# Kernel tuning notes

Hardware: AMD Instinct MI355X
Metric: run time of the kernel (lower is better)

The kernel has to match this reference:

```python
import jax, jax.numpy as jnp
import numpy as np

B, S, D, E, TOP_K = 4, 4096, 2048, 64, 2


def setup_inputs() -> dict:
    key = jax.random.key(0)
    kx, kw, kb = jax.random.split(key, 3)
    x = jax.random.normal(kx, (B, S, D), dtype=jnp.float32)
    # nn.Linear(d_model, n_expert): weight (E, D), bias (E,)
    bound = 1.0 / np.sqrt(D)
    W = jax.random.uniform(kw, (E, D), dtype=jnp.float32, minval=-bound, maxval=bound)
    b = jax.random.uniform(kb, (E,), dtype=jnp.float32, minval=-bound, maxval=bound)
    return {"x": x, "W": W, "b": b}


def reference(x, W, b):
    # logits: (B, S, E)
    logits = jnp.einsum("bsd,ed->bse", x, W) + b
    top_k_logits, ids = jax.lax.top_k(logits, TOP_K)  # (B,S,K) each
    # scatter top-k logits into a -inf filled tensor along the expert dim
    n = B * S
    flat = jnp.full((n, E), -jnp.inf, dtype=logits.dtype)
    rows = jnp.arange(n)[:, None]  # (n,1)
    flat = flat.at[rows, ids.reshape(n, TOP_K)].set(top_k_logits.reshape(n, TOP_K))
    sparse_logits = flat.reshape(B, S, E)
    router_output = jax.nn.softmax(sparse_logits, axis=-1)  # zeros outside top-k
    return router_output, ids
```

## Files before the change

### kernel.cpp

```cpp
#include <hip/hip_runtime.h>
#include <math.h>

#define NTOK 16384
#define D_   2048
#define E_   64
#define TPB  16
#define NKC  (D_/32)

typedef _Float16 f16x8 __attribute__((ext_vector_type(8)));
typedef float    f32x4 __attribute__((ext_vector_type(4)));

#define LSCALE      256.0f
#define LSCALE2_INV (1.0f/65536.0f)

__global__ __launch_bounds__(256)
void prep_w(const float* __restrict__ W,
            _Float16* __restrict__ wh, _Float16* __restrict__ wl)
{
    const int idx = blockIdx.x * 256 + threadIdx.x;
    const int l  = idx & 63;
    const int kc = (idx >> 6) & 63;
    const int nt = idx >> 12;
    const int e  = nt * 16 + (l & 15);
    const int g  = l >> 4;
    const float* src = W + (size_t)e * D_ + kc * 32 + g * 4;
    const float4 f0 = *reinterpret_cast<const float4*>(src);
    const float4 f1 = *reinterpret_cast<const float4*>(src + 16);
    const float v[8] = {f0.x, f0.y, f0.z, f0.w, f1.x, f1.y, f1.z, f1.w};
    f16x8 h, lo;
#pragma unroll
    for (int j = 0; j < 8; ++j) {
        const float vs = v[j] * LSCALE;
        const _Float16 hj = (_Float16)vs;
        h[j]  = hj;
        lo[j] = (_Float16)(vs - (float)hj);
    }
    *reinterpret_cast<f16x8*>(wh + (size_t)idx * 8) = h;
    *reinterpret_cast<f16x8*>(wl + (size_t)idx * 8) = lo;
}

__global__ __launch_bounds__(64, 1)
void router_mfma(const float* __restrict__ x,
                 const _Float16* __restrict__ wh,
                 const _Float16* __restrict__ wl,
                 const float* __restrict__ bias,
                 float* __restrict__ out)
{
    __shared__ float smem[TPB * 65 + TPB * 4];

    const int l  = threadIdx.x;
    const int T0 = blockIdx.x * TPB;
    const int g  = l >> 4;

    const float* xp = x + (size_t)(T0 + (l & 15)) * D_ + g * 4;
    const _Float16* bh_b = wh + (size_t)l * 8;
    const _Float16* bl_b = wl + (size_t)l * 8;

    f32x4 acc0 = {0.f,0.f,0.f,0.f}, acc1 = {0.f,0.f,0.f,0.f};
    f32x4 acc2 = {0.f,0.f,0.f,0.f}, acc3 = {0.f,0.f,0.f,0.f};

    float4 xa[4], xb[4];
    f16x8  BH[4][4], BL[4][4];

#pragma unroll
    for (int j = 0; j < 4; ++j) {
        xa[j] = *reinterpret_cast<const float4*>(xp + j * 32);
        xb[j] = *reinterpret_cast<const float4*>(xp + j * 32 + 16);
#pragma unroll
        for (int nt = 0; nt < 4; ++nt) {
            BH[j][nt] = *reinterpret_cast<const f16x8*>(bh_b + nt * 32768 + j * 512);
            BL[j][nt] = *reinterpret_cast<const f16x8*>(bl_b + nt * 32768 + j * 512);
        }
    }

    for (int s = 0; s < 16; ++s) {
        const int K = s << 2;
#pragma unroll
        for (int j = 0; j < 4; ++j) {
            f16x8 ah, al_;
            {
                float vs;
                vs = xa[j].x * LSCALE; ah[0] = (_Float16)vs; al_[0] = (_Float16)(vs - (float)ah[0]);
                vs = xa[j].y * LSCALE; ah[1] = (_Float16)vs; al_[1] = (_Float16)(vs - (float)ah[1]);
                vs = xa[j].z * LSCALE; ah[2] = (_Float16)vs; al_[2] = (_Float16)(vs - (float)ah[2]);
                vs = xa[j].w * LSCALE; ah[3] = (_Float16)vs; al_[3] = (_Float16)(vs - (float)ah[3]);
                vs = xb[j].x * LSCALE; ah[4] = (_Float16)vs; al_[4] = (_Float16)(vs - (float)ah[4]);
                vs = xb[j].y * LSCALE; ah[5] = (_Float16)vs; al_[5] = (_Float16)(vs - (float)ah[5]);
                vs = xb[j].z * LSCALE; ah[6] = (_Float16)vs; al_[6] = (_Float16)(vs - (float)ah[6]);
                vs = xb[j].w * LSCALE; ah[7] = (_Float16)vs; al_[7] = (_Float16)(vs - (float)ah[7]);
            }
            acc0 = __builtin_amdgcn_mfma_f32_16x16x32_f16(ah,  BH[j][0], acc0, 0, 0, 0);
            acc0 = __builtin_amdgcn_mfma_f32_16x16x32_f16(al_, BH[j][0], acc0, 0, 0, 0);
            acc0 = __builtin_amdgcn_mfma_f32_16x16x32_f16(ah,  BL[j][0], acc0, 0, 0, 0);
            acc1 = __builtin_amdgcn_mfma_f32_16x16x32_f16(ah,  BH[j][1], acc1, 0, 0, 0);
            acc1 = __builtin_amdgcn_mfma_f32_16x16x32_f16(al_, BH[j][1], acc1, 0, 0, 0);
            acc1 = __builtin_amdgcn_mfma_f32_16x16x32_f16(ah,  BL[j][1], acc1, 0, 0, 0);
            acc2 = __builtin_amdgcn_mfma_f32_16x16x32_f16(ah,  BH[j][2], acc2, 0, 0, 0);
            acc2 = __builtin_amdgcn_mfma_f32_16x16x32_f16(al_, BH[j][2], acc2, 0, 0, 0);
            acc2 = __builtin_amdgcn_mfma_f32_16x16x32_f16(ah,  BL[j][2], acc2, 0, 0, 0);
            acc3 = __builtin_amdgcn_mfma_f32_16x16x32_f16(ah,  BH[j][3], acc3, 0, 0, 0);
            acc3 = __builtin_amdgcn_mfma_f32_16x16x32_f16(al_, BH[j][3], acc3, 0, 0, 0);
            acc3 = __builtin_amdgcn_mfma_f32_16x16x32_f16(ah,  BL[j][3], acc3, 0, 0, 0);
            if (s < 15) {
                const int kn = K + j + 4;
                xa[j] = *reinterpret_cast<const float4*>(xp + kn * 32);
                xb[j] = *reinterpret_cast<const float4*>(xp + kn * 32 + 16);
#pragma unroll
                for (int nt = 0; nt < 4; ++nt) {
                    BH[j][nt] = *reinterpret_cast<const f16x8*>(bh_b + nt * 32768 + (size_t)kn * 512);
                    BL[j][nt] = *reinterpret_cast<const f16x8*>(bl_b + nt * 32768 + (size_t)kn * 512);
                }
            }
        }
    }

    {
        const int col = l & 15;
#pragma unroll
        for (int r = 0; r < 4; ++r) {
            const int t = g * 4 + r;
            smem[t * 65 + 0  + col] = acc0[r] * LSCALE2_INV;
            smem[t * 65 + 16 + col] = acc1[r] * LSCALE2_INV;
            smem[t * 65 + 32 + col] = acc2[r] * LSCALE2_INV;
            smem[t * 65 + 48 + col] = acc3[r] * LSCALE2_INV;
        }
    }
    __syncthreads();

    float* res = smem + TPB * 65;
    if (l < TPB) {
        const float* lg = smem + l * 65;
        float m1 = -INFINITY, m2 = -INFINITY;
        int i1 = 0, i2 = 0;
        for (int e = 0; e < E_; ++e) {
            const float v = lg[e] + bias[e];
            if (v > m1)      { m2 = m1; i2 = i1; m1 = v; i1 = e; }
            else if (v > m2) { m2 = v;  i2 = e; }
        }
        const float ex  = expf(m2 - m1);
        const float den = 1.f + ex;
        res[l*4+0] = 1.f / den;
        res[l*4+1] = ex / den;
        res[l*4+2] = (float)i1;
        res[l*4+3] = (float)i2;
    }
    __syncthreads();

    float* ob = out + (size_t)T0 * E_;
#pragma unroll
    for (int i = 0; i < 4; ++i) {
        const int idx = i * 256 + l * 4;
        const int t   = idx >> 6;
        const int e0  = idx & 63;
        const float p1 = res[t*4+0];
        const float p2 = res[t*4+1];
        const int   i1 = (int)res[t*4+2];
        const int   i2 = (int)res[t*4+3];
        float4 v;
        v.x = (e0+0 == i1) ? p1 : ((e0+0 == i2) ? p2 : 0.f);
        v.y = (e0+1 == i1) ? p1 : ((e0+1 == i2) ? p2 : 0.f);
        v.z = (e0+2 == i1) ? p1 : ((e0+2 == i2) ? p2 : 0.f);
        v.w = (e0+3 == i1) ? p1 : ((e0+3 == i2) ? p2 : 0.f);
        *reinterpret_cast<float4*>(ob + idx) = v;
    }
    if (l < TPB * 2) {
        out[(size_t)NTOK * E_ + (size_t)T0 * 2 + l] =
            res[(l >> 1) * 4 + 2 + (l & 1)];
    }
}

extern "C" void kernel_launch(void* const* d_in, const int* in_sizes, int n_in,
                              void* d_out, int out_size, void* d_ws, size_t ws_size,
                              hipStream_t stream) {
    const float* x = (const float*)d_in[0];
    const float* W = (const float*)d_in[1];
    const float* b = (const float*)d_in[2];
    float* out     = (float*)d_out;
    _Float16* wh   = (_Float16*)d_ws;
    _Float16* wl   = wh + (size_t)4 * NKC * 64 * 8;

    hipLaunchKernelGGL(prep_w, dim3(64), dim3(256), 0, stream, W, wh, wl);
    hipLaunchKernelGGL(router_mfma, dim3(NTOK / TPB), dim3(64), 0, stream,
                       x, wh, wl, b, out);
}
```

Baseline: 51.60 us.

## Split expert tiles across four waves per block instead of one wave

Each block now has four wavefronts, and each wave computes one 16-expert column tile for the block's 16 tokens instead of a single wave computing all four tiles. This cuts per-thread register use (fewer B fragments and accumulators) and raises parallelism per token block. In exchange, every wave reloads and re-splits the same x rows, so x traffic from L1/L2 and conversion work become four times larger. The last loop iteration is peeled so the prefetch no longer needs a branch.

```diff
diff --git a/kernel.cpp b/kernel.cpp
--- a/kernel.cpp
+++ b/kernel.cpp
@@ -39,7 +39,7 @@
     *reinterpret_cast<f16x8*>(wl + (size_t)idx * 8) = lo;
 }
 
-__global__ __launch_bounds__(64, 1)
+__global__ __launch_bounds__(256, 4)
 void router_mfma(const float* __restrict__ x,
                  const _Float16* __restrict__ wh,
                  const _Float16* __restrict__ wl,
@@ -48,32 +48,30 @@
 {
     __shared__ float smem[TPB * 65 + TPB * 4];
 
-    const int l  = threadIdx.x;
-    const int T0 = blockIdx.x * TPB;
-    const int g  = l >> 4;
+    const int tid = threadIdx.x;
+    const int l   = tid & 63;
+    const int w   = __builtin_amdgcn_readfirstlane(tid >> 6);
+    const int T0  = blockIdx.x * TPB;
+    const int g   = l >> 4;
 
     const float* xp = x + (size_t)(T0 + (l & 15)) * D_ + g * 4;
-    const _Float16* bh_b = wh + (size_t)l * 8;
-    const _Float16* bl_b = wl + (size_t)l * 8;
+    const _Float16* bh_b = wh + (size_t)w * 32768 + (size_t)l * 8;
+    const _Float16* bl_b = wl + (size_t)w * 32768 + (size_t)l * 8;
 
-    f32x4 acc0 = {0.f,0.f,0.f,0.f}, acc1 = {0.f,0.f,0.f,0.f};
-    f32x4 acc2 = {0.f,0.f,0.f,0.f}, acc3 = {0.f,0.f,0.f,0.f};
+    f32x4 acc = {0.f, 0.f, 0.f, 0.f};
 
     float4 xa[4], xb[4];
-    f16x8  BH[4][4], BL[4][4];
+    f16x8  BH[4], BL[4];
 
 #pragma unroll
     for (int j = 0; j < 4; ++j) {
         xa[j] = *reinterpret_cast<const float4*>(xp + j * 32);
         xb[j] = *reinterpret_cast<const float4*>(xp + j * 32 + 16);
-#pragma unroll
-        for (int nt = 0; nt < 4; ++nt) {
-            BH[j][nt] = *reinterpret_cast<const f16x8*>(bh_b + nt * 32768 + j * 512);
-            BL[j][nt] = *reinterpret_cast<const f16x8*>(bl_b + nt * 32768 + j * 512);
-        }
+        BH[j] = *reinterpret_cast<const f16x8*>(bh_b + j * 512);
+        BL[j] = *reinterpret_cast<const f16x8*>(bl_b + j * 512);
     }
 
-    for (int s = 0; s < 16; ++s) {
+    for (int s = 0; s < 15; ++s) {
         const int K = s << 2;
 #pragma unroll
         for (int j = 0; j < 4; ++j) {
@@ -89,47 +87,48 @@
                 vs = xb[j].z * LSCALE; ah[6] = (_Float16)vs; al_[6] = (_Float16)(vs - (float)ah[6]);
                 vs = xb[j].w * LSCALE; ah[7] = (_Float16)vs; al_[7] = (_Float16)(vs - (float)ah[7]);
             }
-            acc0 = __builtin_amdgcn_mfma_f32_16x16x32_f16(ah,  BH[j][0], acc0, 0, 0, 0);
-            acc0 = __builtin_amdgcn_mfma_f32_16x16x32_f16(al_, BH[j][0], acc0, 0, 0, 0);
-            acc0 = __builtin_amdgcn_mfma_f32_16x16x32_f16(ah,  BL[j][0], acc0, 0, 0, 0);
-            acc1 = __builtin_amdgcn_mfma_f32_16x16x32_f16(ah,  BH[j][1], acc1, 0, 0, 0);
-            acc1 = __builtin_amdgcn_mfma_f32_16x16x32_f16(al_, BH[j][1], acc1, 0, 0, 0);
-            acc1 = __builtin_amdgcn_mfma_f32_16x16x32_f16(ah,  BL[j][1], acc1, 0, 0, 0);
-            acc2 = __builtin_amdgcn_mfma_f32_16x16x32_f16(ah,  BH[j][2], acc2, 0, 0, 0);
-            acc2 = __builtin_amdgcn_mfma_f32_16x16x32_f16(al_, BH[j][2], acc2, 0, 0, 0);
-            acc2 = __builtin_amdgcn_mfma_f32_16x16x32_f16(ah,  BL[j][2], acc2, 0, 0, 0);
-            acc3 = __builtin_amdgcn_mfma_f32_16x16x32_f16(ah,  BH[j][3], acc3, 0, 0, 0);
-            acc3 = __builtin_amdgcn_mfma_f32_16x16x32_f16(al_, BH[j][3], acc3, 0, 0, 0);
-            acc3 = __builtin_amdgcn_mfma_f32_16x16x32_f16(ah,  BL[j][3], acc3, 0, 0, 0);
-            if (s < 15) {
-                const int kn = K + j + 4;
-                xa[j] = *reinterpret_cast<const float4*>(xp + kn * 32);
-                xb[j] = *reinterpret_cast<const float4*>(xp + kn * 32 + 16);
+            acc = __builtin_amdgcn_mfma_f32_16x16x32_f16(ah,  BH[j], acc, 0, 0, 0);
+            acc = __builtin_amdgcn_mfma_f32_16x16x32_f16(al_, BH[j], acc, 0, 0, 0);
+            acc = __builtin_amdgcn_mfma_f32_16x16x32_f16(ah,  BL[j], acc, 0, 0, 0);
+            const int kn = K + j + 4;
+            xa[j] = *reinterpret_cast<const float4*>(xp + kn * 32);
+            xb[j] = *reinterpret_cast<const float4*>(xp + kn * 32 + 16);
+            BH[j] = *reinterpret_cast<const f16x8*>(bh_b + (size_t)kn * 512);
+            BL[j] = *reinterpret_cast<const f16x8*>(bl_b + (size_t)kn * 512);
+        }
+    }
 #pragma unroll
-                for (int nt = 0; nt < 4; ++nt) {
-                    BH[j][nt] = *reinterpret_cast<const f16x8*>(bh_b + nt * 32768 + (size_t)kn * 512);
-                    BL[j][nt] = *reinterpret_cast<const f16x8*>(bl_b + nt * 32768 + (size_t)kn * 512);
-                }
-            }
+    for (int j = 0; j < 4; ++j) {
+        f16x8 ah, al_;
+        {
+            float vs;
+            vs = xa[j].x * LSCALE; ah[0] = (_Float16)vs; al_[0] = (_Float16)(vs - (float)ah[0]);
+            vs = xa[j].y * LSCALE; ah[1] = (_Float16)vs; al_[1] = (_Float16)(vs - (float)ah[1]);
+            vs = xa[j].z * LSCALE; ah[2] = (_Float16)vs; al_[2] = (_Float16)(vs - (float)ah[2]);
+            vs = xa[j].w * LSCALE; ah[3] = (_Float16)vs; al_[3] = (_Float16)(vs - (float)ah[3]);
+            vs = xb[j].x * LSCALE; ah[4] = (_Float16)vs; al_[4] = (_Float16)(vs - (float)ah[4]);
+            vs = xb[j].y * LSCALE; ah[5] = (_Float16)vs; al_[5] = (_Float16)(vs - (float)ah[5]);
+            vs = xb[j].z * LSCALE; ah[6] = (_Float16)vs; al_[6] = (_Float16)(vs - (float)ah[6]);
+            vs = xb[j].w * LSCALE; ah[7] = (_Float16)vs; al_[7] = (_Float16)(vs - (float)ah[7]);
         }
+        acc = __builtin_amdgcn_mfma_f32_16x16x32_f16(ah,  BH[j], acc, 0, 0, 0);
+        acc = __builtin_amdgcn_mfma_f32_16x16x32_f16(al_, BH[j], acc, 0, 0, 0);
+        acc = __builtin_amdgcn_mfma_f32_16x16x32_f16(ah,  BL[j], acc, 0, 0, 0);
     }
 
     {
-        const int col = l & 15;
+        const int col = w * 16 + (l & 15);
 #pragma unroll
         for (int r = 0; r < 4; ++r) {
             const int t = g * 4 + r;
-            smem[t * 65 + 0  + col] = acc0[r] * LSCALE2_INV;
-            smem[t * 65 + 16 + col] = acc1[r] * LSCALE2_INV;
-            smem[t * 65 + 32 + col] = acc2[r] * LSCALE2_INV;
-            smem[t * 65 + 48 + col] = acc3[r] * LSCALE2_INV;
+            smem[t * 65 + col] = acc[r] * LSCALE2_INV;
         }
     }
     __syncthreads();
 
     float* res = smem + TPB * 65;
-    if (l < TPB) {
-        const float* lg = smem + l * 65;
+    if (tid < TPB) {
+        const float* lg = smem + tid * 65;
         float m1 = -INFINITY, m2 = -INFINITY;
         int i1 = 0, i2 = 0;
         for (int e = 0; e < E_; ++e) {
@@ -139,17 +138,16 @@
         }
         const float ex  = expf(m2 - m1);
         const float den = 1.f + ex;
-        res[l*4+0] = 1.f / den;
-        res[l*4+1] = ex / den;
-        res[l*4+2] = (float)i1;
-        res[l*4+3] = (float)i2;
+        res[tid*4+0] = 1.f / den;
+        res[tid*4+1] = ex / den;
+        res[tid*4+2] = (float)i1;
+        res[tid*4+3] = (float)i2;
     }
     __syncthreads();
 
     float* ob = out + (size_t)T0 * E_;
-#pragma unroll
-    for (int i = 0; i < 4; ++i) {
-        const int idx = i * 256 + l * 4;
+    {
+        const int idx = tid * 4;
         const int t   = idx >> 6;
         const int e0  = idx & 63;
         const float p1 = res[t*4+0];
@@ -163,9 +161,9 @@
         v.w = (e0+3 == i1) ? p1 : ((e0+3 == i2) ? p2 : 0.f);
         *reinterpret_cast<float4*>(ob + idx) = v;
     }
-    if (l < TPB * 2) {
-        out[(size_t)NTOK * E_ + (size_t)T0 * 2 + l] =
-            res[(l >> 1) * 4 + 2 + (l & 1)];
+    if (tid < TPB * 2) {
+        out[(size_t)NTOK * E_ + (size_t)T0 * 2 + tid] =
+            res[(tid >> 1) * 4 + 2 + (tid & 1)];
     }
 }
 
@@ -180,6 +178,6 @@
     _Float16* wl   = wh + (size_t)4 * NKC * 64 * 8;
 
     hipLaunchKernelGGL(prep_w, dim3(64), dim3(256), 0, stream, W, wh, wl);
-    hipLaunchKernelGGL(router_mfma, dim3(NTOK / TPB), dim3(64), 0, stream,
+    hipLaunchKernelGGL(router_mfma, dim3(NTOK / TPB), dim3(256), 0, stream,
                        x, wh, wl, b, out);
 }
```

Result: slower. 94.30 us (+82.7%).
